# Kernel optimization log

Hardware: AMD Instinct MI355X
Metric: run time of the kernel (lower is better)

Reference implementation:

```python
import jax, jax.numpy as jnp
import numpy as np

COMMITMENT_COST = 0.25
NUM_EMBEDDINGS = 8192
EMBEDDING_DIM = 256


def setup_inputs() -> dict:
    key = jax.random.key(0)
    kx, ke = jax.random.split(key)
    x = jax.random.normal(kx, (16, 1024, EMBEDDING_DIM), dtype=jnp.float32)
    # nn.Embedding weight initialized uniform(-1/K, 1/K)
    embedding = jax.random.uniform(
        ke, (NUM_EMBEDDINGS, EMBEDDING_DIM), dtype=jnp.float32,
        minval=-1.0 / NUM_EMBEDDINGS, maxval=1.0 / NUM_EMBEDDINGS)
    return {"x": x, "embedding": embedding}


def reference(x, embedding):
    x_shape = x.shape
    D = embedding.shape[1]
    K = embedding.shape[0]
    flat_x = x.reshape(-1, D)                      # [N, D]
    N = flat_x.shape[0]

    distances = (jnp.sum(flat_x ** 2, axis=1, keepdims=True)
                 + jnp.sum(embedding ** 2, axis=1)
                 - 2.0 * jnp.matmul(flat_x, embedding.T))
    encoding_indices = jnp.argmin(distances, axis=1)  # [N]

    # one-hot @ embedding == gather
    quantized = embedding[encoding_indices].reshape(x_shape)

    sg = jax.lax.stop_gradient
    e_latent_loss = jnp.mean((sg(quantized) - x) ** 2)
    q_latent_loss = jnp.mean((quantized - sg(x)) ** 2)
    loss = q_latent_loss + COMMITMENT_COST * e_latent_loss

    # straight-through estimator
    quantized_st = x + sg(quantized - x)

    # perplexity from mean one-hot usage
    counts = jnp.zeros((K,), dtype=jnp.float32).at[encoding_indices].add(1.0)
    avg_probs = counts / N
    perplexity = jnp.exp(-jnp.sum(avg_probs * jnp.log(avg_probs + 1e-10)))

    return quantized_st.reshape(x_shape), loss, perplexity
```

## Files before the change

### kernel.cpp

```cpp
#include <hip/hip_runtime.h>


#define VQ_N 16384
#define VQ_D 256
#define VQ_K 8192

typedef __attribute__((ext_vector_type(8))) short short8;
typedef __attribute__((ext_vector_type(4))) float f32x4;

__device__ inline unsigned short f2bf(float f) {
  unsigned int u = __float_as_uint(f);
  return (unsigned short)((u + 0x7fffu + ((u >> 16) & 1u)) >> 16);
}

__global__ __launch_bounds__(256) void vq_pack_e(
    const float* __restrict__ E, unsigned short* __restrict__ Ebs,
    float* __restrict__ enorm) {
  const int gid = blockIdx.x * 256 + threadIdx.x;
  const int k = gid >> 5;
  const int g = gid & 31;
  const float* src = E + (size_t)k * VQ_D + g * 8;
  const float4 a = *(const float4*)src;
  const float4 b = *(const float4*)(src + 4);
  uint4 o;
  o.x = (unsigned)f2bf(a.x) | ((unsigned)f2bf(a.y) << 16);
  o.y = (unsigned)f2bf(a.z) | ((unsigned)f2bf(a.w) << 16);
  o.z = (unsigned)f2bf(b.x) | ((unsigned)f2bf(b.y) << 16);
  o.w = (unsigned)f2bf(b.z) | ((unsigned)f2bf(b.w) << 16);
  const size_t off = ((size_t)(k >> 5) * 1024 + (size_t)g * 32 + (k & 31)) * 8;
  *(uint4*)(Ebs + off) = o;
  double s = (double)a.x * a.x + (double)a.y * a.y + (double)a.z * a.z +
             (double)a.w * a.w + (double)b.x * b.x + (double)b.y * b.y +
             (double)b.z * b.z + (double)b.w * b.w;
#pragma unroll
  for (int m = 1; m <= 16; m <<= 1) s += __shfl_xor(s, m, 64);
  if (g == 0) enorm[k] = (float)s;
}

__global__ __launch_bounds__(256, 1) void vq_score_argmin(
    const float* __restrict__ X, const unsigned short* __restrict__ Ebs,
    const float* __restrict__ enorm,
    int* __restrict__ indices, int* __restrict__ counts) {
  __shared__ float red_s[4][64];
  __shared__ int red_i[4][64];

  const int tid = threadIdx.x;
  const int wave = tid >> 6;
  const int lane = tid & 63;
  const int quad = lane >> 4;
  const int c15 = lane & 15;
  const int r0 = blockIdx.x * 64;

  short8 af[4][8];
#pragma unroll
  for (int t = 0; t < 4; ++t) {
    const float* xr = X + (size_t)(r0 + t * 16 + c15) * VQ_D + quad * 8;
#pragma unroll
    for (int kb = 0; kb < 8; ++kb) {
      const float4 a = *(const float4*)(xr + kb * 32);
      const float4 b = *(const float4*)(xr + kb * 32 + 4);
      short8 f;
      f[0] = (short)f2bf(a.x); f[1] = (short)f2bf(a.y);
      f[2] = (short)f2bf(a.z); f[3] = (short)f2bf(a.w);
      f[4] = (short)f2bf(b.x); f[5] = (short)f2bf(b.y);
      f[6] = (short)f2bf(b.z); f[7] = (short)f2bf(b.w);
      af[t][kb] = f;
    }
  }

  float best_s[4][4];
  int best_i[4][4];
#pragma unroll
  for (int t = 0; t < 4; ++t)
#pragma unroll
    for (int r = 0; r < 4; ++r) { best_s[t][r] = 3.4e38f; best_i[t][r] = 0; }

  const unsigned short* ebase = Ebs + (size_t)quad * 256 + (size_t)c15 * 8;

#define LOADB(buf, en, gg)                                                   \
  {                                                                          \
    const unsigned short* bp =                                               \
        ebase + (size_t)((gg) >> 1) * 8192 + (size_t)((gg)&1) * 128;         \
    _Pragma("unroll") for (int kb = 0; kb < 8; ++kb)                         \
        buf[kb] = *(const short8*)(bp + kb * 1024);                          \
    en = enorm[(gg)*16 + c15];                                               \
  }

#define COMPUTE(buf, en, gg)                                                 \
  {                                                                          \
    f32x4 a0 = {0.f, 0.f, 0.f, 0.f}, a1 = {0.f, 0.f, 0.f, 0.f};             \
    f32x4 a2 = {0.f, 0.f, 0.f, 0.f}, a3 = {0.f, 0.f, 0.f, 0.f};             \
    _Pragma("unroll") for (int kb = 0; kb < 8; ++kb) {                       \
      a0 = __builtin_amdgcn_mfma_f32_16x16x32_bf16(af[0][kb], buf[kb], a0, 0, 0, 0); \
      a1 = __builtin_amdgcn_mfma_f32_16x16x32_bf16(af[1][kb], buf[kb], a1, 0, 0, 0); \
      a2 = __builtin_amdgcn_mfma_f32_16x16x32_bf16(af[2][kb], buf[kb], a2, 0, 0, 0); \
      a3 = __builtin_amdgcn_mfma_f32_16x16x32_bf16(af[3][kb], buf[kb], a3, 0, 0, 0); \
    }                                                                        \
    const int code = (gg)*16 + c15;                                          \
    _Pragma("unroll") for (int r = 0; r < 4; ++r) {                          \
      float s;                                                               \
      s = fmaf(a0[r], -2.0f, en);                                            \
      if (s < best_s[0][r]) { best_s[0][r] = s; best_i[0][r] = code; }       \
      s = fmaf(a1[r], -2.0f, en);                                            \
      if (s < best_s[1][r]) { best_s[1][r] = s; best_i[1][r] = code; }       \
      s = fmaf(a2[r], -2.0f, en);                                            \
      if (s < best_s[2][r]) { best_s[2][r] = s; best_i[2][r] = code; }       \
      s = fmaf(a3[r], -2.0f, en);                                            \
      if (s < best_s[3][r]) { best_s[3][r] = s; best_i[3][r] = code; }       \
    }                                                                        \
  }

  short8 bb0[8], bb1[8];
  float en0, en1;
  LOADB(bb0, en0, wave);
  for (int it = 0; it < 128; it += 2) {
    const int g0 = wave + 4 * it;
    LOADB(bb1, en1, g0 + 4);
    COMPUTE(bb0, en0, g0);
    if (it + 2 < 128) LOADB(bb0, en0, g0 + 8);
    COMPUTE(bb1, en1, g0 + 4);
  }
#undef LOADB
#undef COMPUTE

#pragma unroll
  for (int t = 0; t < 4; ++t)
#pragma unroll
    for (int r = 0; r < 4; ++r) {
      float s = best_s[t][r];
      int i = best_i[t][r];
#pragma unroll
      for (int m = 1; m <= 8; m <<= 1) {
        const float os = __shfl_xor(s, m, 64);
        const int oi = __shfl_xor(i, m, 64);
        if (os < s || (os == s && oi < i)) { s = os; i = oi; }
      }
      if (c15 == 0) {
        red_s[wave][t * 16 + quad * 4 + r] = s;
        red_i[wave][t * 16 + quad * 4 + r] = i;
      }
    }
  __syncthreads();

  if (tid < 64) {
    float bs = red_s[0][tid];
    int bi = red_i[0][tid];
#pragma unroll
    for (int w = 1; w < 4; ++w) {
      const float s = red_s[w][tid];
      const int i = red_i[w][tid];
      if (s < bs || (s == bs && i < bi)) { bs = s; bi = i; }
    }
    indices[r0 + tid] = bi;
    atomicAdd(&counts[bi], 1);
  }
}

__global__ __launch_bounds__(256) void vq_gather_loss(
    const float* __restrict__ X, const float* __restrict__ E,
    const int* __restrict__ indices, float* __restrict__ outq,
    double* __restrict__ loss_sum) {
  __shared__ double wsum[4];
  const int wid = threadIdx.x >> 6;
  const int lane = threadIdx.x & 63;
  const int gw = blockIdx.x * 4 + wid;
  double acc = 0.0;
#pragma unroll 4
  for (int row = gw; row < VQ_N; row += 2048) {
    const int k = indices[row];
    const float4 q = *(const float4*)(E + (size_t)k * VQ_D + lane * 4);
    const float4 x = *(const float4*)(X + (size_t)row * VQ_D + lane * 4);
    *(float4*)(outq + (size_t)row * VQ_D + lane * 4) = q;
    const double dx = (double)q.x - x.x, dy = (double)q.y - x.y;
    const double dz = (double)q.z - x.z, dw = (double)q.w - x.w;
    acc += dx * dx + dy * dy + dz * dz + dw * dw;
  }
#pragma unroll
  for (int off = 32; off > 0; off >>= 1) acc += __shfl_down(acc, off, 64);
  if (lane == 0) wsum[wid] = acc;
  __syncthreads();
  if (threadIdx.x == 0)
    atomicAdd(loss_sum, wsum[0] + wsum[1] + wsum[2] + wsum[3]);
}

__global__ __launch_bounds__(256) void vq_finalize(
    const int* __restrict__ counts, const double* __restrict__ loss_sum,
    float* __restrict__ out) {
  __shared__ double part[256];
  const int tx = threadIdx.x;
  double s = 0.0;
  for (int k = tx; k < VQ_K; k += 256) {
    const int c = counts[k];
    if (c > 0) {
      const double p = (double)c * (1.0 / (double)VQ_N);
      s += p * log(p + 1e-10);
    }
  }
  part[tx] = s;
  __syncthreads();
  for (int off = 128; off > 0; off >>= 1) {
    if (tx < off) part[tx] += part[tx + off];
    __syncthreads();
  }
  if (tx == 0) {
    out[(size_t)VQ_N * VQ_D] =
        (float)(1.25 * (*loss_sum) / ((double)VQ_N * (double)VQ_D));
    out[(size_t)VQ_N * VQ_D + 1] = (float)exp(-part[0]);
  }
}

extern "C" void kernel_launch(void* const* d_in, const int* in_sizes, int n_in,
                              void* d_out, int out_size, void* d_ws,
                              size_t ws_size, hipStream_t stream) {
  const float* X = (const float*)d_in[0];
  const float* E = (const float*)d_in[1];
  float* out = (float*)d_out;

  char* ws = (char*)d_ws;
  unsigned short* Ebs = (unsigned short*)ws;
  float* enorm = (float*)(ws + 4194304);
  double* loss_sum = (double*)(ws + 4227072);
  int* counts = (int*)(ws + 4227136);
  int* indices = (int*)(ws + 4259904);

  hipMemsetAsync(ws + 4227072, 0, 64 + 32768, stream);

  vq_pack_e<<<1024, 256, 0, stream>>>(E, Ebs, enorm);
  vq_score_argmin<<<256, 256, 0, stream>>>(X, Ebs, enorm, indices, counts);
  vq_gather_loss<<<512, 256, 0, stream>>>(X, E, indices, out, loss_sum);
  vq_finalize<<<1, 256, 0, stream>>>(counts, loss_sum, out);
}
```

Measured before the change: 186.1 us.

## Split codebook across two blocks per row tile and merge argmin downstream

The score/argmin kernel now launches two blocks per 64-row tile, each scanning half of the codebook, and writes a packed (orderable distance, index) 64-bit key per half. The gather kernel merges the two halves with a min on the packed keys. The histogram moves into the single-block finalize kernel as a shared-memory histogram, and the memset is replaced by zeroing loss_sum inside the pack kernel. The aim is to fill more of the GPU's compute units (256 blocks was under one per CU) at the cost of loading the X fragments twice and a serial histogram pass in one block.

```diff
diff --git a/kernel.cpp b/kernel.cpp
--- a/kernel.cpp
+++ b/kernel.cpp
@@ -13,10 +13,16 @@
   return (unsigned short)((u + 0x7fffu + ((u >> 16) & 1u)) >> 16);
 }
 
+__device__ inline unsigned int orderable(float s) {
+  const unsigned int u = __float_as_uint(s);
+  return ((int)u < 0) ? ~u : (u | 0x80000000u);
+}
+
 __global__ __launch_bounds__(256) void vq_pack_e(
     const float* __restrict__ E, unsigned short* __restrict__ Ebs,
-    float* __restrict__ enorm) {
+    float* __restrict__ enorm, double* __restrict__ loss_sum) {
   const int gid = blockIdx.x * 256 + threadIdx.x;
+  if (gid == 0) *loss_sum = 0.0;
   const int k = gid >> 5;
   const int g = gid & 31;
   const float* src = E + (size_t)k * VQ_D + g * 8;
@@ -37,10 +43,9 @@
   if (g == 0) enorm[k] = (float)s;
 }
 
-__global__ __launch_bounds__(256, 1) void vq_score_argmin(
+__global__ __launch_bounds__(256, 2) void vq_score_argmin(
     const float* __restrict__ X, const unsigned short* __restrict__ Ebs,
-    const float* __restrict__ enorm,
-    int* __restrict__ indices, int* __restrict__ counts) {
+    const float* __restrict__ enorm, unsigned long long* __restrict__ best64) {
   __shared__ float red_s[4][64];
   __shared__ int red_i[4][64];
 
@@ -49,7 +54,9 @@
   const int lane = tid & 63;
   const int quad = lane >> 4;
   const int c15 = lane & 15;
-  const int r0 = blockIdx.x * 64;
+  const int rowblk = blockIdx.x >> 1;
+  const int half = blockIdx.x & 1;
+  const int r0 = rowblk * 64;
 
   short8 af[4][8];
 #pragma unroll
@@ -110,14 +117,15 @@
     }                                                                        \
   }
 
+  const int gbase = half * 256 + wave;
   short8 bb0[8], bb1[8];
   float en0, en1;
-  LOADB(bb0, en0, wave);
-  for (int it = 0; it < 128; it += 2) {
-    const int g0 = wave + 4 * it;
+  LOADB(bb0, en0, gbase);
+  for (int it = 0; it < 64; it += 2) {
+    const int g0 = gbase + 4 * it;
     LOADB(bb1, en1, g0 + 4);
     COMPUTE(bb0, en0, g0);
-    if (it + 2 < 128) LOADB(bb0, en0, g0 + 8);
+    if (it + 2 < 64) LOADB(bb0, en0, g0 + 8);
     COMPUTE(bb1, en1, g0 + 4);
   }
 #undef LOADB
@@ -151,14 +159,14 @@
       const int i = red_i[w][tid];
       if (s < bs || (s == bs && i < bi)) { bs = s; bi = i; }
     }
-    indices[r0 + tid] = bi;
-    atomicAdd(&counts[bi], 1);
+    best64[(size_t)half * VQ_N + r0 + tid] =
+        ((unsigned long long)orderable(bs) << 32) | (unsigned)bi;
   }
 }
 
 __global__ __launch_bounds__(256) void vq_gather_loss(
     const float* __restrict__ X, const float* __restrict__ E,
-    const int* __restrict__ indices, float* __restrict__ outq,
+    const unsigned long long* __restrict__ best64, float* __restrict__ outq,
     double* __restrict__ loss_sum) {
   __shared__ double wsum[4];
   const int wid = threadIdx.x >> 6;
@@ -167,7 +175,10 @@
   double acc = 0.0;
 #pragma unroll 4
   for (int row = gw; row < VQ_N; row += 2048) {
-    const int k = indices[row];
+    const unsigned long long p0 = best64[row];
+    const unsigned long long p1 = best64[VQ_N + row];
+    const unsigned long long p = (p1 < p0) ? p1 : p0;
+    const int k = (int)(p & 0xFFFFFFFFu);
     const float4 q = *(const float4*)(E + (size_t)k * VQ_D + lane * 4);
     const float4 x = *(const float4*)(X + (size_t)row * VQ_D + lane * 4);
     *(float4*)(outq + (size_t)row * VQ_D + lane * 4) = q;
@@ -184,16 +195,26 @@
 }
 
 __global__ __launch_bounds__(256) void vq_finalize(
-    const int* __restrict__ counts, const double* __restrict__ loss_sum,
-    float* __restrict__ out) {
+    const unsigned long long* __restrict__ best64,
+    const double* __restrict__ loss_sum, float* __restrict__ out) {
+  __shared__ int hist[VQ_K];
   __shared__ double part[256];
   const int tx = threadIdx.x;
+  for (int k = tx; k < VQ_K; k += 256) hist[k] = 0;
+  __syncthreads();
+  for (int row = tx; row < VQ_N; row += 256) {
+    const unsigned long long p0 = best64[row];
+    const unsigned long long p1 = best64[VQ_N + row];
+    const unsigned long long p = (p1 < p0) ? p1 : p0;
+    atomicAdd(&hist[(int)(p & 0xFFFFFFFFu)], 1);
+  }
+  __syncthreads();
   double s = 0.0;
   for (int k = tx; k < VQ_K; k += 256) {
-    const int c = counts[k];
+    const int c = hist[k];
     if (c > 0) {
-      const double p = (double)c * (1.0 / (double)VQ_N);
-      s += p * log(p + 1e-10);
+      const double pr = (double)c * (1.0 / (double)VQ_N);
+      s += pr * log(pr + 1e-10);
     }
   }
   part[tx] = s;
@@ -220,13 +241,11 @@
   unsigned short* Ebs = (unsigned short*)ws;
   float* enorm = (float*)(ws + 4194304);
   double* loss_sum = (double*)(ws + 4227072);
-  int* counts = (int*)(ws + 4227136);
-  int* indices = (int*)(ws + 4259904);
-
-  hipMemsetAsync(ws + 4227072, 0, 64 + 32768, stream);
-
-  vq_pack_e<<<1024, 256, 0, stream>>>(E, Ebs, enorm);
-  vq_score_argmin<<<256, 256, 0, stream>>>(X, Ebs, enorm, indices, counts);
-  vq_gather_loss<<<512, 256, 0, stream>>>(X, E, indices, out, loss_sum);
-  vq_finalize<<<1, 256, 0, stream>>>(counts, loss_sum, out);
-}
+  unsigned long long* best64 =
+      (unsigned long long*)(ws + 4227136);
+
+  vq_pack_e<<<1024, 256, 0, stream>>>(E, Ebs, enorm, loss_sum);
+  vq_score_argmin<<<512, 256, 0, stream>>>(X, Ebs, enorm, best64);
+  vq_gather_loss<<<512, 256, 0, stream>>>(X, E, best64, out, loss_sum);
+  vq_finalize<<<1, 256, 0, stream>>>(best64, loss_sum, out);
+}
```

Measured after the change: 213.7 us. 14.8% more time.
